# Performance work log

Measured on AMD Instinct MI355X. Metric: run time of the kernel, lower is better.

The kernel has to match this reference:

```python
import jax, jax.numpy as jnp
import numpy as np

B, V, T = 512, 50257, 2048   # batch, vocab, history length
TOP_K = 50                    # from __init__ arg top_k
NEG_INF = jnp.float32(-1e30)  # finite stand-in for -inf (same softmax result, clean grads)


def setup_inputs() -> dict:
    key = jax.random.key(0)
    k1, k2, k3 = jax.random.split(key, 3)
    logits = jax.random.normal(k1, (B, V), jnp.float32) * 4.0
    previous_tokens = jax.random.randint(k2, (B, T), 0, V)
    # uniform noise for the Gumbel-max trick (torch.rand_like); avoid log(0)
    rand_u = jax.random.uniform(k3, (B, V), jnp.float32, minval=1e-10, maxval=1.0)
    return {
        "logits": logits,
        "previous_tokens": previous_tokens,
        "rand_u": rand_u,
        "temperature": jnp.full((1, 1), 0.8, jnp.float32),
        "top_p": jnp.full((1, 1), 0.8, jnp.float32),
        "repetition_penalty": jnp.full((1, 1), 1.35, jnp.float32),
    }


def _logits_to_probs(logits, previous_tokens, temperature, top_p, repetition_penalty):
    b = jnp.arange(logits.shape[0])[:, None]
    # repetition penalty: gather scores at previous tokens, rescale, scatter back
    score = jnp.take_along_axis(logits, previous_tokens, axis=1)            # [B, T]
    score = jnp.where(score < 0, score * repetition_penalty, score / repetition_penalty)
    logits = logits.at[b, previous_tokens].set(score)
    # top-p (nucleus) filtering: sort descending, cumulative softmax mass
    order = jnp.argsort(-logits, axis=-1)                                   # [B, V]
    sorted_logits = jnp.take_along_axis(logits, order, axis=1)
    cum_probs = jnp.cumsum(jax.nn.softmax(sorted_logits, axis=-1), axis=-1)
    remove_sorted = cum_probs > top_p
    remove_sorted = remove_sorted.at[:, 0].set(False)                       # always keep best token
    # unsort the removal mask back to vocab order (order is a permutation)
    remove = jnp.zeros_like(remove_sorted).at[b, order].set(remove_sorted)
    logits = jnp.where(remove, NEG_INF, logits)
    # temperature
    logits = logits / jnp.maximum(temperature, 1e-5)
    # top-k filtering: mask everything below the k-th largest logit
    v = jax.lax.top_k(logits, TOP_K)[0]                                     # [B, TOP_K]
    pivot = v[:, -1:]
    logits = jnp.where(logits < pivot, NEG_INF, logits)
    return jax.nn.softmax(logits, axis=-1)


def reference(logits, previous_tokens, rand_u, temperature, top_p, repetition_penalty):
    probs = _logits_to_probs(logits, previous_tokens, temperature, top_p, repetition_penalty)
    # Gumbel-max multinomial sample: argmax(probs / Exp(1))
    q = -jnp.log(rand_u)
    idx_next = jnp.argmax(probs / q, axis=-1, keepdims=True).astype(jnp.int64)
    return idx_next, probs
```

## Files before the change

kernel.cpp:

```cpp
#include <hip/hip_runtime.h>
#include <cstdint>
#include <cmath>

#define V_SIZE 50257
#define T_SIZE 2048
#define B_SIZE 512
#define NTHR 1024
#define NWAVE (NTHR / 64)
#define CAND_MAX 1024
#define SPEC_THRESH 10.0f
#define SPEC_MIN 80
#define KOFF 32.0f

extern "C" __global__ __launch_bounds__(NTHR, 8)
void decode_kernel(const float* __restrict__ logits,
                   const int*   __restrict__ prev,
                   const float* __restrict__ rand_u,
                   const float* __restrict__ tempp,
                   const float* __restrict__ toppp,
                   const float* __restrict__ repp,
                   float* __restrict__ out)
{
    const int row  = blockIdx.x;
    const int tid  = threadIdx.x;
    const int lane = tid & 63;
    const int wid  = tid >> 6;

    __shared__ unsigned int bitmap[(V_SIZE + 31) / 32];
    __shared__ float cval[CAND_MAX];
    __shared__ int   cidx[CAND_MAX];
    __shared__ float rbuf[CAND_MAX];
    __shared__ float redf[NWAVE];
    __shared__ int   redi[NWAVE];
    __shared__ float sM, sZ, sS;
    __shared__ int   sCnt, sSend;

    const float rp   = repp[0];
    const float topp = toppp[0];
    const float temp = fmaxf(tempp[0], 1e-5f);

    const size_t rowoff = (size_t)row * V_SIZE;
    const float* lrow = logits + rowoff;
    const float* urow = rand_u + rowoff;
    float*       orow = out + B_SIZE + rowoff;

    for (int i = tid; i < (V_SIZE + 31) / 32; i += NTHR) bitmap[i] = 0u;
    if (tid == 0) sCnt = 0;
    __syncthreads();

    const int4* prow4 = (const int4*)(prev + (size_t)row * T_SIZE);
    for (int i = tid; i < T_SIZE / 4; i += NTHR) {
        int4 t = prow4[i];
        atomicOr(&bitmap[((unsigned)t.x) >> 5], 1u << (t.x & 31));
        atomicOr(&bitmap[((unsigned)t.y) >> 5], 1u << (t.y & 31));
        atomicOr(&bitmap[((unsigned)t.z) >> 5], 1u << (t.z & 31));
        atomicOr(&bitmap[((unsigned)t.w) >> 5], 1u << (t.w & 31));
    }
    __syncthreads();

    const int head  = (4 - (row & 3)) & 3;
    const int nvec  = (V_SIZE - head) >> 2;
    const int tails = head + nvec * 4;
    const float4* lrow4 = (const float4*)(lrow + head);

    float lm = -INFINITY, lz = 0.0f;
    auto process1 = [&](float x, int v) {
        unsigned w = bitmap[v >> 5];
        if ((w >> (v & 31)) & 1u) x = (x < 0.0f) ? x * rp : x / rp;
        if (x > SPEC_THRESH) {
            int p = atomicAdd(&sCnt, 1);
            if (p < CAND_MAX) { cval[p] = x; cidx[p] = v; }
        }
        lm = fmaxf(lm, x);
        lz += __expf(x - KOFF);
    };
    if (tid < head)           process1(lrow[tid], tid);
    if (tid < V_SIZE - tails) process1(lrow[tails + tid], tails + tid);
    for (int i = tid; i < nvec; i += NTHR) {
        float4 x4 = lrow4[i];
        int v = head + i * 4;
        process1(x4.x, v); process1(x4.y, v + 1);
        process1(x4.z, v + 2); process1(x4.w, v + 3);
    }

    {
        float wm = lm;
        for (int off = 32; off; off >>= 1) wm = fmaxf(wm, __shfl_down(wm, off));
        if (lane == 0) redf[wid] = wm;
    }
    __syncthreads();
    if (tid == 0) {
        float m = redf[0];
        for (int i = 1; i < NWAVE; ++i) m = fmaxf(m, redf[i]);
        sM = m;
    }
    __syncthreads();
    const float M = sM;

    {
        float wz = lz;
        for (int off = 32; off; off >>= 1) wz += __shfl_down(wz, off);
        if (lane == 0) redf[wid] = wz;
    }
    __syncthreads();
    if (tid == 0) {
        float s = 0.0f;
        for (int i = 0; i < NWAVE; ++i) s += redf[i];
        sZ = s * expf(KOFF - M);
    }
    __syncthreads();
    const float Z = sZ;

    int cnt = sCnt;
    int C;
    if (cnt >= SPEC_MIN && cnt <= CAND_MAX) {
        C = cnt;
    } else {
        auto count_pass = [&](float thr) -> int {
            __syncthreads();
            if (tid == 0) sCnt = 0;
            __syncthreads();
            int local = 0;
            for (int v = tid; v < V_SIZE; v += NTHR) {
                float x = lrow[v];
                unsigned w = bitmap[v >> 5];
                if ((w >> (v & 31)) & 1u) x = (x < 0.0f) ? x * rp : x / rp;
                if (x > thr) local++;
            }
            if (local) atomicAdd(&sCnt, local);
            __syncthreads();
            return sCnt;
        };
        float a = -200.0f, b = 200.0f, thr = 0.0f;
        int c = 0;
        for (int it = 0; it < 40; ++it) {
            thr = 0.5f * (a + b);
            c = count_pass(thr);
            if (c < SPEC_MIN)       b = thr;
            else if (c > CAND_MAX)  a = thr;
            else break;
        }
        if (c < SPEC_MIN) thr = a;
        __syncthreads();
        if (tid == 0) sCnt = 0;
        __syncthreads();
        for (int v = tid; v < V_SIZE; v += NTHR) {
            float x = lrow[v];
            unsigned w = bitmap[v >> 5];
            if ((w >> (v & 31)) & 1u) x = (x < 0.0f) ? x * rp : x / rp;
            if (x > thr) {
                int p = atomicAdd(&sCnt, 1);
                if (p < CAND_MAX) { cval[p] = x; cidx[p] = v; }
            }
        }
        __syncthreads();
        C = min(sCnt, CAND_MAX);
    }

    int n = 1; while (n < C) n <<= 1;
    for (int i = C + tid; i < n; i += NTHR) { cval[i] = -INFINITY; cidx[i] = 0x7FFFFFFF; }
    __syncthreads();
    for (int k = 2; k <= n; k <<= 1) {
        for (int j = k >> 1; j > 0; j >>= 1) {
            for (int i = tid; i < n; i += NTHR) {
                int l = i ^ j;
                if (l > i) {
                    float vi = cval[i], vl = cval[l];
                    int   ii = cidx[i], il = cidx[l];
                    bool lFirst = (vl > vi) || (vl == vi && il < ii);
                    bool asc = ((i & k) == 0);
                    if (lFirst == asc) {
                        cval[i] = vl; cval[l] = vi;
                        cidx[i] = il; cidx[l] = ii;
                    }
                }
            }
            __syncthreads();
        }
    }

    if (tid == 0) {
        float cum = 0.0f;
        int m = 0;
        float vp = cval[min(49, C - 1)];
        for (int i = 0; i < C; ++i) {
            cum += expf(cval[i] - M) / Z;
            if (i > 0 && cum > topp) break;
            m = i;
            if (m >= 49 && cval[i] < vp) break;
        }
        int send;
        if (m >= 49) {
            int e = 49;
            while (e + 1 < C && cval[e + 1] == vp) ++e;
            send = (m < e) ? m : e;
        } else {
            send = m;
        }
        sSend = send;
    }
    __syncthreads();

    const int send = sSend;
    const float v0 = cval[0];
    for (int i = tid; i <= send; i += NTHR)
        rbuf[i] = expf(cval[i] / temp - v0 / temp);
    __syncthreads();
    if (tid == 0) {
        float S = 0.0f;
        for (int i = 0; i <= send; ++i) S += rbuf[i];
        sS = S;
    }
    __syncthreads();
    const float S = sS;

    float bestr = -1.0f;
    int   besti = 0x7FFFFFFF;
    for (int i = tid; i <= send; i += NTHR) {
        float p = rbuf[i] / S;
        int v = cidx[i];
        orow[v] = p;
        float q = -logf(urow[v]);
        float r = p / q;
        if (r > bestr || (r == bestr && v < besti)) { bestr = r; besti = v; }
    }
    for (int off = 32; off; off >>= 1) {
        float r2 = __shfl_down(bestr, off);
        int   i2 = __shfl_down(besti, off);
        if (r2 > bestr || (r2 == bestr && i2 < besti)) { bestr = r2; besti = i2; }
    }
    if (lane == 0) { redf[wid] = bestr; redi[wid] = besti; }
    __syncthreads();
    if (tid == 0) {
        float br = redf[0]; int bi = redi[0];
        for (int i = 1; i < NWAVE; ++i) {
            if (redf[i] > br || (redf[i] == br && redi[i] < bi)) { br = redf[i]; bi = redi[i]; }
        }
        out[row] = (float)bi;
    }
}

extern "C" void kernel_launch(void* const* d_in, const int* in_sizes, int n_in,
                              void* d_out, int out_size, void* d_ws, size_t ws_size,
                              hipStream_t stream) {
    const float* logits = (const float*)d_in[0];
    const int*   prev   = (const int*)d_in[1];
    const float* rand_u = (const float*)d_in[2];
    const float* tempp  = (const float*)d_in[3];
    const float* toppp  = (const float*)d_in[4];
    const float* repp   = (const float*)d_in[5];
    float* out = (float*)d_out;

    hipMemsetAsync(d_out, 0, (size_t)out_size * sizeof(float), stream);

    hipLaunchKernelGGL(decode_kernel, dim3(B_SIZE), dim3(NTHR), 0, stream,
                       logits, prev, rand_u, tempp, toppp, repp, out);
}
```

Before: 262.0 us.

## Split decode into streaming pass and decide kernel using output scratch

Splits the single kernel into two. The first is a streaming pass that collects candidates from the raw logits and builds the softmax denominator, applying the repetition-penalty correction only to the unique previous tokens. The second kernel reloads candidates from scratch space in the output row, then sorts, filters and samples with 512 threads. The goal is to remove the per-element bitmap lookup from the main stream and shrink the serial sort/select tail. In exchange it adds a second launch plus a global scratch round-trip and zeroing step, and its fast path collects candidates on pre-penalty values, which could miss tokens in rare edge cases.

Measured after the change: 264.3 us. No clear change (+0.9%).

```diff
diff --git a/kernel.cpp b/kernel.cpp
--- a/kernel.cpp
+++ b/kernel.cpp
@@ -5,15 +5,122 @@
 #define V_SIZE 50257
 #define T_SIZE 2048
 #define B_SIZE 512
-#define NTHR 1024
-#define NWAVE (NTHR / 64)
 #define CAND_MAX 1024
 #define SPEC_THRESH 10.0f
 #define SPEC_MIN 80
 #define KOFF 32.0f
 
-extern "C" __global__ __launch_bounds__(NTHR, 8)
-void decode_kernel(const float* __restrict__ logits,
+#define NTHR1 1024
+#define NWAVE1 (NTHR1 / 64)
+#define NTHR2 512
+#define NWAVE2 (NTHR2 / 64)
+
+#define BM_WORDS ((V_SIZE + 31) / 32)
+
+#define SCR_BASE (V_SIZE - (2 * CAND_MAX + 2))
+#define SCR_VALS (SCR_BASE)
+#define SCR_IDX  (SCR_BASE + CAND_MAX)
+#define SCR_CNT  (SCR_BASE + 2 * CAND_MAX)
+#define SCR_STOT (SCR_BASE + 2 * CAND_MAX + 1)
+
+extern "C" __global__ __launch_bounds__(NTHR1, 8)
+void pass1_kernel(const float* __restrict__ logits,
+                  const int*   __restrict__ prev,
+                  const float* __restrict__ repp,
+                  float* __restrict__ out)
+{
+    const int row  = blockIdx.x;
+    const int tid  = threadIdx.x;
+    const int lane = tid & 63;
+    const int wid  = tid >> 6;
+
+    __shared__ unsigned int bitmap[BM_WORDS];
+    __shared__ float cval[CAND_MAX];
+    __shared__ int   cidx[CAND_MAX];
+    __shared__ float redf[NWAVE1];
+    __shared__ int   sCnt;
+
+    const float rp = repp[0];
+    const float* lrow = logits + (size_t)row * V_SIZE;
+    float*       orow = out + B_SIZE + (size_t)row * V_SIZE;
+
+    for (int i = tid; i < BM_WORDS; i += NTHR1) bitmap[i] = 0u;
+    if (tid == 0) sCnt = 0;
+    __syncthreads();
+
+    const int* prow = prev + (size_t)row * T_SIZE;
+    float corr = 0.0f;
+    for (int i = tid; i < T_SIZE; i += NTHR1) {
+        int v = prow[i];
+        unsigned bit = 1u << (v & 31);
+        unsigned old = atomicOr(&bitmap[((unsigned)v) >> 5], bit);
+        if (!(old & bit)) {
+            float x  = lrow[v];
+            float xp = (x < 0.0f) ? x * rp : x / rp;
+            corr += __expf(xp - KOFF) - __expf(x - KOFF);
+        }
+    }
+
+    const int head  = (4 - (row & 3)) & 3;
+    const int nvec  = (V_SIZE - head) >> 2;
+    const int tails = head + nvec * 4;
+    const float4* lrow4 = (const float4*)(lrow + head);
+
+    float lz0 = 0.0f, lz1 = 0.0f;
+    auto collect = [&](float x, int v) {
+        if (x > SPEC_THRESH) {
+            int p = atomicAdd(&sCnt, 1);
+            if (p < CAND_MAX) { cval[p] = x; cidx[p] = v; }
+        }
+    };
+    if (tid < head) {
+        float x = lrow[tid];
+        collect(x, tid);
+        lz0 += __expf(x - KOFF);
+    }
+    if (tid < V_SIZE - tails) {
+        float x = lrow[tails + tid];
+        collect(x, tails + tid);
+        lz0 += __expf(x - KOFF);
+    }
+    for (int i = tid; i < nvec; i += NTHR1) {
+        float4 x4 = lrow4[i];
+        int v = head + i * 4;
+        collect(x4.x, v);     collect(x4.y, v + 1);
+        collect(x4.z, v + 2); collect(x4.w, v + 3);
+        lz0 += __expf(x4.x - KOFF) + __expf(x4.z - KOFF);
+        lz1 += __expf(x4.y - KOFF) + __expf(x4.w - KOFF);
+    }
+    __syncthreads();
+
+    const int C = min(sCnt, CAND_MAX);
+    for (int i = tid; i < C; i += NTHR1) {
+        int v = cidx[i];
+        if ((bitmap[((unsigned)v) >> 5] >> (v & 31)) & 1u) {
+            float x = cval[i];
+            cval[i] = (x < 0.0f) ? x * rp : x / rp;
+        }
+    }
+
+    float wz = lz0 + lz1 + corr;
+    for (int off = 32; off; off >>= 1) wz += __shfl_down(wz, off);
+    if (lane == 0) redf[wid] = wz;
+    __syncthreads();
+
+    for (int i = tid; i < C; i += NTHR1) {
+        orow[SCR_VALS + i] = cval[i];
+        orow[SCR_IDX  + i] = __int_as_float(cidx[i]);
+    }
+    if (tid == 0) {
+        float s = 0.0f;
+        for (int i = 0; i < NWAVE1; ++i) s += redf[i];
+        orow[SCR_CNT]  = __int_as_float(sCnt);
+        orow[SCR_STOT] = s;
+    }
+}
+
+extern "C" __global__ __launch_bounds__(NTHR2, 8)
+void decide_kernel(const float* __restrict__ logits,
                    const int*   __restrict__ prev,
                    const float* __restrict__ rand_u,
                    const float* __restrict__ tempp,
@@ -26,12 +133,12 @@
     const int lane = tid & 63;
     const int wid  = tid >> 6;
 
-    __shared__ unsigned int bitmap[(V_SIZE + 31) / 32];
+    __shared__ unsigned int bitmap[BM_WORDS];
     __shared__ float cval[CAND_MAX];
     __shared__ int   cidx[CAND_MAX];
     __shared__ float rbuf[CAND_MAX];
-    __shared__ float redf[NWAVE];
-    __shared__ int   redi[NWAVE];
+    __shared__ float redf[NWAVE2];
+    __shared__ int   redi[NWAVE2];
     __shared__ float sM, sZ, sS;
     __shared__ int   sCnt, sSend;
 
@@ -44,87 +151,90 @@
     const float* urow = rand_u + rowoff;
     float*       orow = out + B_SIZE + rowoff;
 
-    for (int i = tid; i < (V_SIZE + 31) / 32; i += NTHR) bitmap[i] = 0u;
-    if (tid == 0) sCnt = 0;
-    __syncthreads();
-
-    const int4* prow4 = (const int4*)(prev + (size_t)row * T_SIZE);
-    for (int i = tid; i < T_SIZE / 4; i += NTHR) {
-        int4 t = prow4[i];
-        atomicOr(&bitmap[((unsigned)t.x) >> 5], 1u << (t.x & 31));
-        atomicOr(&bitmap[((unsigned)t.y) >> 5], 1u << (t.y & 31));
-        atomicOr(&bitmap[((unsigned)t.z) >> 5], 1u << (t.z & 31));
-        atomicOr(&bitmap[((unsigned)t.w) >> 5], 1u << (t.w & 31));
-    }
-    __syncthreads();
-
-    const int head  = (4 - (row & 3)) & 3;
-    const int nvec  = (V_SIZE - head) >> 2;
-    const int tails = head + nvec * 4;
-    const float4* lrow4 = (const float4*)(lrow + head);
-
-    float lm = -INFINITY, lz = 0.0f;
-    auto process1 = [&](float x, int v) {
-        unsigned w = bitmap[v >> 5];
-        if ((w >> (v & 31)) & 1u) x = (x < 0.0f) ? x * rp : x / rp;
-        if (x > SPEC_THRESH) {
-            int p = atomicAdd(&sCnt, 1);
-            if (p < CAND_MAX) { cval[p] = x; cidx[p] = v; }
-        }
-        lm = fmaxf(lm, x);
-        lz += __expf(x - KOFF);
-    };
-    if (tid < head)           process1(lrow[tid], tid);
-    if (tid < V_SIZE - tails) process1(lrow[tails + tid], tails + tid);
-    for (int i = tid; i < nvec; i += NTHR) {
-        float4 x4 = lrow4[i];
-        int v = head + i * 4;
-        process1(x4.x, v); process1(x4.y, v + 1);
-        process1(x4.z, v + 2); process1(x4.w, v + 3);
-    }
-
-    {
-        float wm = lm;
-        for (int off = 32; off; off >>= 1) wm = fmaxf(wm, __shfl_down(wm, off));
-        if (lane == 0) redf[wid] = wm;
-    }
-    __syncthreads();
-    if (tid == 0) {
-        float m = redf[0];
-        for (int i = 1; i < NWAVE; ++i) m = fmaxf(m, redf[i]);
-        sM = m;
-    }
-    __syncthreads();
-    const float M = sM;
-
-    {
-        float wz = lz;
-        for (int off = 32; off; off >>= 1) wz += __shfl_down(wz, off);
-        if (lane == 0) redf[wid] = wz;
-    }
-    __syncthreads();
-    if (tid == 0) {
-        float s = 0.0f;
-        for (int i = 0; i < NWAVE; ++i) s += redf[i];
-        sZ = s * expf(KOFF - M);
-    }
-    __syncthreads();
-    const float Z = sZ;
-
-    int cnt = sCnt;
-    int C;
-    if (cnt >= SPEC_MIN && cnt <= CAND_MAX) {
-        C = cnt;
-    } else {
+    const int   cntRaw = __float_as_int(orow[SCR_CNT]);
+    const float stot   = orow[SCR_STOT];
+
+    int C = 0;
+    float M = 0.0f, Z = 1.0f;
+    bool ok = (cntRaw >= SPEC_MIN && cntRaw <= CAND_MAX);
+
+    if (ok) {
+        C = cntRaw;
+        float lm = -INFINITY;
+        for (int i = tid; i < C; i += NTHR2) {
+            float v = orow[SCR_VALS + i];
+            cval[i] = v;
+            cidx[i] = __float_as_int(orow[SCR_IDX + i]);
+            lm = fmaxf(lm, v);
+        }
+        for (int off = 32; off; off >>= 1) lm = fmaxf(lm, __shfl_down(lm, off));
+        if (lane == 0) redf[wid] = lm;
+        __syncthreads();
+        if (tid == 0) {
+            float m = redf[0];
+            for (int i = 1; i < NWAVE2; ++i) m = fmaxf(m, redf[i]);
+            sM = m;
+        }
+        __syncthreads();
+        M = sM;
+        Z = stot * expf(KOFF - M);
+        if (!(M > SPEC_THRESH)) ok = false;
+    }
+
+    if (!ok) {
+        for (int i = tid; i < BM_WORDS; i += NTHR2) bitmap[i] = 0u;
+        __syncthreads();
+        const int* prow = prev + (size_t)row * T_SIZE;
+        for (int i = tid; i < T_SIZE; i += NTHR2) {
+            int v = prow[i];
+            atomicOr(&bitmap[((unsigned)v) >> 5], 1u << (v & 31));
+        }
+        __syncthreads();
+
+        float lm = -INFINITY, lz = 0.0f;
+        for (int v = tid; v < V_SIZE; v += NTHR2) {
+            float x = lrow[v];
+            if ((bitmap[((unsigned)v) >> 5] >> (v & 31)) & 1u)
+                x = (x < 0.0f) ? x * rp : x / rp;
+            lm = fmaxf(lm, x);
+            lz += __expf(x - KOFF);
+        }
+        {
+            float wm = lm;
+            for (int off = 32; off; off >>= 1) wm = fmaxf(wm, __shfl_down(wm, off));
+            if (lane == 0) redf[wid] = wm;
+        }
+        __syncthreads();
+        if (tid == 0) {
+            float m = redf[0];
+            for (int i = 1; i < NWAVE2; ++i) m = fmaxf(m, redf[i]);
+            sM = m;
+        }
+        __syncthreads();
+        M = sM;
+        {
+            float wz = lz;
+            for (int off = 32; off; off >>= 1) wz += __shfl_down(wz, off);
+            if (lane == 0) redf[wid] = wz;
+        }
+        __syncthreads();
+        if (tid == 0) {
+            float s = 0.0f;
+            for (int i = 0; i < NWAVE2; ++i) s += redf[i];
+            sZ = s * expf(KOFF - M);
+        }
+        __syncthreads();
+        Z = sZ;
+
         auto count_pass = [&](float thr) -> int {
             __syncthreads();
             if (tid == 0) sCnt = 0;
             __syncthreads();
             int local = 0;
-            for (int v = tid; v < V_SIZE; v += NTHR) {
+            for (int v = tid; v < V_SIZE; v += NTHR2) {
                 float x = lrow[v];
-                unsigned w = bitmap[v >> 5];
-                if ((w >> (v & 31)) & 1u) x = (x < 0.0f) ? x * rp : x / rp;
+                if ((bitmap[((unsigned)v) >> 5] >> (v & 31)) & 1u)
+                    x = (x < 0.0f) ? x * rp : x / rp;
                 if (x > thr) local++;
             }
             if (local) atomicAdd(&sCnt, local);
@@ -144,10 +254,10 @@
         __syncthreads();
         if (tid == 0) sCnt = 0;
         __syncthreads();
-        for (int v = tid; v < V_SIZE; v += NTHR) {
+        for (int v = tid; v < V_SIZE; v += NTHR2) {
             float x = lrow[v];
-            unsigned w = bitmap[v >> 5];
-            if ((w >> (v & 31)) & 1u) x = (x < 0.0f) ? x * rp : x / rp;
+            if ((bitmap[((unsigned)v) >> 5] >> (v & 31)) & 1u)
+                x = (x < 0.0f) ? x * rp : x / rp;
             if (x > thr) {
                 int p = atomicAdd(&sCnt, 1);
                 if (p < CAND_MAX) { cval[p] = x; cidx[p] = v; }
@@ -157,12 +267,15 @@
         C = min(sCnt, CAND_MAX);
     }
 
+    for (int i = tid; i < 2 * CAND_MAX + 2; i += NTHR2)
+        orow[SCR_BASE + i] = 0.0f;
+
     int n = 1; while (n < C) n <<= 1;
-    for (int i = C + tid; i < n; i += NTHR) { cval[i] = -INFINITY; cidx[i] = 0x7FFFFFFF; }
+    for (int i = C + tid; i < n; i += NTHR2) { cval[i] = -INFINITY; cidx[i] = 0x7FFFFFFF; }
     __syncthreads();
     for (int k = 2; k <= n; k <<= 1) {
         for (int j = k >> 1; j > 0; j >>= 1) {
-            for (int i = tid; i < n; i += NTHR) {
+            for (int i = tid; i < n; i += NTHR2) {
                 int l = i ^ j;
                 if (l > i) {
                     float vi = cval[i], vl = cval[l];
@@ -179,12 +292,16 @@
         }
     }
 
+    for (int i = tid; i < C; i += NTHR2)
+        rbuf[i] = expf(cval[i] - M) / Z;
+    __syncthreads();
+
     if (tid == 0) {
         float cum = 0.0f;
         int m = 0;
         float vp = cval[min(49, C - 1)];
         for (int i = 0; i < C; ++i) {
-            cum += expf(cval[i] - M) / Z;
+            cum += rbuf[i];
             if (i > 0 && cum > topp) break;
             m = i;
             if (m >= 49 && cval[i] < vp) break;
@@ -203,7 +320,7 @@
 
     const int send = sSend;
     const float v0 = cval[0];
-    for (int i = tid; i <= send; i += NTHR)
+    for (int i = tid; i <= send; i += NTHR2)
         rbuf[i] = expf(cval[i] / temp - v0 / temp);
     __syncthreads();
     if (tid == 0) {
@@ -216,7 +333,7 @@
 
     float bestr = -1.0f;
     int   besti = 0x7FFFFFFF;
-    for (int i = tid; i <= send; i += NTHR) {
+    for (int i = tid; i <= send; i += NTHR2) {
         float p = rbuf[i] / S;
         int v = cidx[i];
         orow[v] = p;
@@ -233,7 +350,7 @@
     __syncthreads();
     if (tid == 0) {
         float br = redf[0]; int bi = redi[0];
-        for (int i = 1; i < NWAVE; ++i) {
+        for (int i = 1; i < NWAVE2; ++i) {
             if (redf[i] > br || (redf[i] == br && redi[i] < bi)) { br = redf[i]; bi = redi[i]; }
         }
         out[row] = (float)bi;
@@ -251,8 +368,10 @@
     const float* repp   = (const float*)d_in[5];
     float* out = (float*)d_out;
 
-    hipMemsetAsync(d_out, 0, (size_t)out_size * sizeof(float), stream);
-
-    hipLaunchKernelGGL(decode_kernel, dim3(B_SIZE), dim3(NTHR), 0, stream,
+    (void)hipMemsetAsync(d_out, 0, (size_t)out_size * sizeof(float), stream);
+
+    hipLaunchKernelGGL(pass1_kernel, dim3(B_SIZE), dim3(NTHR1), 0, stream,
+                       logits, prev, repp, out);
+    hipLaunchKernelGGL(decide_kernel, dim3(B_SIZE), dim3(NTHR2), 0, stream,
                        logits, prev, rand_u, tempp, toppp, repp, out);
 }
```
